# Kernel optimization log

Measured on AMD Instinct MI355X. Metric: run time of the kernel, lower is better.

Reference implementation:

```python
import jax, jax.numpy as jnp
import numpy as np

BS, S, H, T = 16, 256, 1024, 32  # batch, num entities, hidden, num relation tags
N_TAGS = 7


def setup_inputs() -> dict:
    key = jax.random.key(0)
    k0, k1, k2, k3 = jax.random.split(key, 4)
    seq_embedding = jax.random.normal(k0, (BS, H), dtype=jnp.float32)
    entities_embeddings = jax.random.normal(k1, (BS, S, H), dtype=jnp.float32)
    entities_tags = jax.random.randint(k2, (BS, S), 0, N_TAGS)
    # relation_classifier: Linear(3*H -> T)
    W = jax.random.normal(k3, (T, 3 * H), dtype=jnp.float32) * 0.02
    b = jnp.zeros((T,), dtype=jnp.float32)
    return {
        "seq_embedding": seq_embedding,
        "entities_embeddings": entities_embeddings,
        "W": W,
        "b": b,
        "entities_tags": entities_tags,
    }


def reference(seq_embedding, entities_embeddings, W, b, entities_tags):
    # Original (eval mode, dropout=identity):
    #   pred[b,i,j] = W @ concat(E[b,i], E[b,j], S[b]) + bias
    # (arg1/arg2/all_seq linears and tag embeddings are dead code in the
    #  original forward: their outputs are never used.)
    # Decompose W = [W1 | W2 | W3] along the feature axis; mathematically
    # identical to materializing the (bs,S,S,3H) concat tensor.
    h = entities_embeddings.shape[-1]
    W1, W2, W3 = W[:, :h], W[:, h:2 * h], W[:, 2 * h:]
    p1 = jnp.einsum('bih,th->bit', entities_embeddings, W1)  # arg1 contribution
    p2 = jnp.einsum('bjh,th->bjt', entities_embeddings, W2)  # arg2 contribution
    ps = seq_embedding @ W3.T + b                             # seq + bias
    # (bs, S, S, T)
    return p1[:, :, None, :] + p2[:, None, :, :] + ps[:, None, None, :]
```

## Files before the change

kernel.cpp:

```cpp
#include <hip/hip_runtime.h>

#define BS 16
#define S  256
#define H  1024
#define T  32

#define PS_OFF 0
#define P1_OFF 512
#define P2_OFF (P1_OFF + BS * S * T)

typedef __bf16 bf16x8 __attribute__((ext_vector_type(8)));
typedef float  f32x4  __attribute__((ext_vector_type(4)));

__device__ inline bf16x8 to_bf8(float4 lo, float4 hi) {
    bf16x8 r;
    r[0] = (__bf16)lo.x; r[1] = (__bf16)lo.y; r[2] = (__bf16)lo.z; r[3] = (__bf16)lo.w;
    r[4] = (__bf16)hi.x; r[5] = (__bf16)hi.y; r[6] = (__bf16)hi.z; r[7] = (__bf16)hi.w;
    return r;
}

__global__ __launch_bounds__(256) void gemm_ps(
    const float* __restrict__ seq, const float* __restrict__ E,
    const float* __restrict__ W, const float* __restrict__ bias,
    float* __restrict__ ws)
{
    const int tid = threadIdx.x;
    const int lane = tid & 63, wv = tid >> 6;

    if (blockIdx.x < 128) {
        float* ps = ws + PS_OFF;
        const int o = blockIdx.x * 4 + wv;
        const int bb = o >> 5, t = o & 31;
        const float4* sp = (const float4*)(seq + (size_t)bb * H) + lane * 4;
        const float4* wp = (const float4*)(W + (size_t)t * (3 * H) + 2 * H) + lane * 4;
        float acc = 0.f;
        #pragma unroll
        for (int k = 0; k < 4; ++k) {
            float4 a = sp[k], w = wp[k];
            acc += a.x * w.x + a.y * w.y + a.z * w.z + a.w * w.w;
        }
        #pragma unroll
        for (int m = 32; m >= 1; m >>= 1) acc += __shfl_xor(acc, m);
        if (lane == 0) ps[o] = acc + bias[t];
        return;
    }

    __shared__ __align__(16) __bf16 Ebf[16][1032];
    __shared__ __align__(16) float  pacc[4][16][64];

    const int m0 = (blockIdx.x - 128) * 16;

    #pragma unroll
    for (int i = 0; i < 8; ++i) {
        int f = tid + i * 256;
        int row = f >> 7, c8 = f & 127;
        const float4* src = (const float4*)(E + (size_t)(m0 + row) * H + c8 * 8);
        *(bf16x8*)&Ebf[row][c8 * 8] = to_bf8(src[0], src[1]);
    }

    const int kc = wv * 256;
    const int ksub = (lane >> 4) * 8;
    bf16x8 bf[32];
    #pragma unroll
    for (int nt = 0; nt < 4; ++nt) {
        const int col = nt * 16 + (lane & 15);
        const float* wb = W + (size_t)(col & 31) * (3 * H)
                            + ((col >= 32) ? H : 0) + kc + ksub;
        #pragma unroll
        for (int s = 0; s < 8; ++s)
            bf[nt * 8 + s] = to_bf8(*(const float4*)(wb + s * 32),
                                    *(const float4*)(wb + s * 32 + 4));
    }

    __syncthreads();

    f32x4 acc[4] = {{0.f,0.f,0.f,0.f},{0.f,0.f,0.f,0.f},
                    {0.f,0.f,0.f,0.f},{0.f,0.f,0.f,0.f}};
    const int erow = lane & 15;
    #pragma unroll
    for (int s = 0; s < 8; ++s) {
        bf16x8 a = *(const bf16x8*)&Ebf[erow][kc + s * 32 + ksub];
        acc[0] = __builtin_amdgcn_mfma_f32_16x16x32_bf16(a, bf[s],      acc[0], 0, 0, 0);
        acc[1] = __builtin_amdgcn_mfma_f32_16x16x32_bf16(a, bf[8 + s],  acc[1], 0, 0, 0);
        acc[2] = __builtin_amdgcn_mfma_f32_16x16x32_bf16(a, bf[16 + s], acc[2], 0, 0, 0);
        acc[3] = __builtin_amdgcn_mfma_f32_16x16x32_bf16(a, bf[24 + s], acc[3], 0, 0, 0);
    }

    const int prow = (lane >> 4) * 4;
    #pragma unroll
    for (int nt = 0; nt < 4; ++nt)
        #pragma unroll
        for (int r = 0; r < 4; ++r)
            pacc[wv][prow + r][nt * 16 + (lane & 15)] = acc[nt][r];

    __syncthreads();

    const int col = tid & 63;
    const int r0 = tid >> 6;
    #pragma unroll
    for (int rr = 0; rr < 4; ++rr) {
        const int row = r0 + rr * 4;
        float v = (pacc[0][row][col] + pacc[1][row][col])
                + (pacc[2][row][col] + pacc[3][row][col]);
        if (col < 32) (ws + P1_OFF)[(size_t)(m0 + row) * T + col] = v;
        else          (ws + P2_OFF)[(size_t)(m0 + row) * T + (col - 32)] = v;
    }
}

__global__ __launch_bounds__(256) void bcast_add(
    const float* __restrict__ ws, float* __restrict__ out)
{
    const int blk = blockIdx.x;
    const int b = blk >> 8, i = blk & 255;
    const int tid = threadIdx.x;

    __shared__ __align__(16) float s1[32];
    if (tid < 32)
        s1[tid] = (ws + P1_OFF)[(size_t)(b * S + i) * T + tid]
                + (ws + PS_OFF)[b * T + tid];
    __syncthreads();

    const float4 s = *(const float4*)&s1[(tid & 7) * 4];
    const float4* p2v = (const float4*)(ws + P2_OFF) + (size_t)b * (S * T / 4);
    float4* ov = (float4*)out + (size_t)(b * S + i) * (S * T / 4);

    #pragma unroll
    for (int k = tid; k < S * T / 4; k += 256) {
        float4 v = p2v[k];
        float4 r;
        r.x = v.x + s.x; r.y = v.y + s.y; r.z = v.z + s.z; r.w = v.w + s.w;
        ov[k] = r;
    }
}

extern "C" void kernel_launch(void* const* d_in, const int* in_sizes, int n_in,
                              void* d_out, int out_size, void* d_ws, size_t ws_size,
                              hipStream_t stream)
{
    const float* seq  = (const float*)d_in[0];
    const float* E    = (const float*)d_in[1];
    const float* W    = (const float*)d_in[2];
    const float* bias = (const float*)d_in[3];
    float* out = (float*)d_out;
    float* ws  = (float*)d_ws;

    gemm_ps<<<384, 256, 0, stream>>>(seq, E, W, bias, ws);
    bcast_add<<<BS * S, 256, 0, stream>>>(ws, out);
}
```

Baseline: 43.66 us.

## Widen GEMM blocks to 16 waves, drop shared staging, use nontemporal stores

The projection kernel now runs 1024-thread blocks: 16 waves split the work as 4 K-slices by 4 column groups, so each wave holds only 8 B fragments and issues a single MFMA chain, which cuts register pressure. The grid shrinks to 288 blocks. The broadcast kernel reads its row vector straight from global memory instead of staging it through shared memory with a barrier, and writes the large output with nontemporal stores to avoid polluting the cache. Larger blocks may reduce occupancy flexibility, and the output write dominates the total time, so the gain is likely small.

Result: faster. 40.68 us (-6.8%).

```diff
diff --git a/kernel.cpp b/kernel.cpp
--- a/kernel.cpp
+++ b/kernel.cpp
@@ -11,6 +11,7 @@
 
 typedef __bf16 bf16x8 __attribute__((ext_vector_type(8)));
 typedef float  f32x4  __attribute__((ext_vector_type(4)));
+typedef float  f4n    __attribute__((ext_vector_type(4)));
 
 __device__ inline bf16x8 to_bf8(float4 lo, float4 hi) {
     bf16x8 r;
@@ -19,7 +20,7 @@
     return r;
 }
 
-__global__ __launch_bounds__(256) void gemm_ps(
+__global__ __launch_bounds__(1024) void gemm_ps(
     const float* __restrict__ seq, const float* __restrict__ E,
     const float* __restrict__ W, const float* __restrict__ bias,
     float* __restrict__ ws)
@@ -27,9 +28,9 @@
     const int tid = threadIdx.x;
     const int lane = tid & 63, wv = tid >> 6;
 
-    if (blockIdx.x < 128) {
+    if (blockIdx.x < 32) {
         float* ps = ws + PS_OFF;
-        const int o = blockIdx.x * 4 + wv;
+        const int o = blockIdx.x * 16 + wv;
         const int bb = o >> 5, t = o & 31;
         const float4* sp = (const float4*)(seq + (size_t)bb * H) + lane * 4;
         const float4* wp = (const float4*)(W + (size_t)t * (3 * H) + 2 * H) + lane * 4;
@@ -48,62 +49,51 @@
     __shared__ __align__(16) __bf16 Ebf[16][1032];
     __shared__ __align__(16) float  pacc[4][16][64];
 
-    const int m0 = (blockIdx.x - 128) * 16;
+    const int m0 = (blockIdx.x - 32) * 16;
+    const int ks = wv >> 2;
+    const int cg = wv & 3;
+    const int kbeg = ks * 256;
+
+    const int col = cg * 16 + (lane & 15);
+    const int ksub = (lane >> 4) * 8;
+    const float* wbase = W + (size_t)(col & 31) * (3 * H)
+                           + ((col >= 32) ? H : 0) + kbeg + ksub;
+    bf16x8 bfrag[8];
+    #pragma unroll
+    for (int s = 0; s < 8; ++s)
+        bfrag[s] = to_bf8(*(const float4*)(wbase + s * 32),
+                          *(const float4*)(wbase + s * 32 + 4));
 
     #pragma unroll
-    for (int i = 0; i < 8; ++i) {
-        int f = tid + i * 256;
-        int row = f >> 7, c8 = f & 127;
+    for (int i = 0; i < 2; ++i) {
+        int c = tid + i * 1024;
+        int row = c >> 7, c8 = c & 127;
         const float4* src = (const float4*)(E + (size_t)(m0 + row) * H + c8 * 8);
         *(bf16x8*)&Ebf[row][c8 * 8] = to_bf8(src[0], src[1]);
     }
+    __syncthreads();
 
-    const int kc = wv * 256;
-    const int ksub = (lane >> 4) * 8;
-    bf16x8 bf[32];
+    f32x4 acc = {0.f, 0.f, 0.f, 0.f};
+    const int erow = lane & 15;
+    const int kof = kbeg + ksub;
     #pragma unroll
-    for (int nt = 0; nt < 4; ++nt) {
-        const int col = nt * 16 + (lane & 15);
-        const float* wb = W + (size_t)(col & 31) * (3 * H)
-                            + ((col >= 32) ? H : 0) + kc + ksub;
-        #pragma unroll
-        for (int s = 0; s < 8; ++s)
-            bf[nt * 8 + s] = to_bf8(*(const float4*)(wb + s * 32),
-                                    *(const float4*)(wb + s * 32 + 4));
+    for (int s = 0; s < 8; ++s) {
+        bf16x8 a = *(const bf16x8*)&Ebf[erow][kof + s * 32];
+        acc = __builtin_amdgcn_mfma_f32_16x16x32_bf16(a, bfrag[s], acc, 0, 0, 0);
     }
 
+    const int orow = (lane >> 4) * 4;
+    #pragma unroll
+    for (int r = 0; r < 4; ++r)
+        pacc[ks][orow + r][col] = acc[r];
     __syncthreads();
 
-    f32x4 acc[4] = {{0.f,0.f,0.f,0.f},{0.f,0.f,0.f,0.f},
-                    {0.f,0.f,0.f,0.f},{0.f,0.f,0.f,0.f}};
-    const int erow = lane & 15;
-    #pragma unroll
-    for (int s = 0; s < 8; ++s) {
-        bf16x8 a = *(const bf16x8*)&Ebf[erow][kc + s * 32 + ksub];
-        acc[0] = __builtin_amdgcn_mfma_f32_16x16x32_bf16(a, bf[s],      acc[0], 0, 0, 0);
-        acc[1] = __builtin_amdgcn_mfma_f32_16x16x32_bf16(a, bf[8 + s],  acc[1], 0, 0, 0);
-        acc[2] = __builtin_amdgcn_mfma_f32_16x16x32_bf16(a, bf[16 + s], acc[2], 0, 0, 0);
-        acc[3] = __builtin_amdgcn_mfma_f32_16x16x32_bf16(a, bf[24 + s], acc[3], 0, 0, 0);
-    }
-
-    const int prow = (lane >> 4) * 4;
-    #pragma unroll
-    for (int nt = 0; nt < 4; ++nt)
-        #pragma unroll
-        for (int r = 0; r < 4; ++r)
-            pacc[wv][prow + r][nt * 16 + (lane & 15)] = acc[nt][r];
-
-    __syncthreads();
-
-    const int col = tid & 63;
-    const int r0 = tid >> 6;
-    #pragma unroll
-    for (int rr = 0; rr < 4; ++rr) {
-        const int row = r0 + rr * 4;
-        float v = (pacc[0][row][col] + pacc[1][row][col])
-                + (pacc[2][row][col] + pacc[3][row][col]);
-        if (col < 32) (ws + P1_OFF)[(size_t)(m0 + row) * T + col] = v;
-        else          (ws + P2_OFF)[(size_t)(m0 + row) * T + (col - 32)] = v;
+    {
+        const int row = tid >> 6, c = tid & 63;
+        float v = (pacc[0][row][c] + pacc[1][row][c])
+                + (pacc[2][row][c] + pacc[3][row][c]);
+        if (c < 32) (ws + P1_OFF)[(size_t)(m0 + row) * T + c] = v;
+        else        (ws + P2_OFF)[(size_t)(m0 + row) * T + (c - 32)] = v;
     }
 }
 
@@ -114,22 +104,22 @@
     const int b = blk >> 8, i = blk & 255;
     const int tid = threadIdx.x;
 
-    __shared__ __align__(16) float s1[32];
-    if (tid < 32)
-        s1[tid] = (ws + P1_OFF)[(size_t)(b * S + i) * T + tid]
-                + (ws + PS_OFF)[b * T + tid];
-    __syncthreads();
+    const float4 s1v = *(const float4*)((ws + P1_OFF)
+                       + (size_t)(b * S + i) * T + (tid & 7) * 4);
+    const float4 psv = *(const float4*)((ws + PS_OFF) + b * T + (tid & 7) * 4);
+    float4 s;
+    s.x = s1v.x + psv.x; s.y = s1v.y + psv.y;
+    s.z = s1v.z + psv.z; s.w = s1v.w + psv.w;
 
-    const float4 s = *(const float4*)&s1[(tid & 7) * 4];
     const float4* p2v = (const float4*)(ws + P2_OFF) + (size_t)b * (S * T / 4);
     float4* ov = (float4*)out + (size_t)(b * S + i) * (S * T / 4);
 
     #pragma unroll
     for (int k = tid; k < S * T / 4; k += 256) {
         float4 v = p2v[k];
-        float4 r;
+        f4n r;
         r.x = v.x + s.x; r.y = v.y + s.y; r.z = v.z + s.z; r.w = v.w + s.w;
-        ov[k] = r;
+        __builtin_nontemporal_store(r, (f4n*)&ov[k]);
     }
 }
 
@@ -144,6 +134,6 @@
     float* out = (float*)d_out;
     float* ws  = (float*)d_ws;
 
-    gemm_ps<<<384, 256, 0, stream>>>(seq, E, W, bias, ws);
+    gemm_ps<<<288, 1024, 0, stream>>>(seq, E, W, bias, ws);
     bcast_add<<<BS * S, 256, 0, stream>>>(ws, out);
 }
```

## Fuse projection GEMM into tiled broadcast-add kernel, dropping p1/p2 workspace round trip

Applied to the files above, without the earlier changes.

Replaces the GEMM-then-broadcast pair with a small ps kernel plus a tiled kernel in which each block recomputes the p1 rows for 16 i and the p2 rows for 64 j of one batch with MFMA. It then writes the 16x64x32 output tile straight from shared memory. This removes the p1/p2 workspace writes and the re-reads of p2 across the broadcast. In exchange E and W are re-read and recomputed redundantly across tiles (each E row is converted about 4x, W is loaded per block), adding extra GEMM work before the store-bound output phase.

New measurement: 135.6 us. 211% more time.

```diff
diff --git a/kernel.cpp b/kernel.cpp
--- a/kernel.cpp
+++ b/kernel.cpp
@@ -4,10 +4,10 @@
 #define S  256
 #define H  1024
 #define T  32
+#define IT 16
+#define JT 64
 
 #define PS_OFF 0
-#define P1_OFF 512
-#define P2_OFF (P1_OFF + BS * S * T)
 
 typedef __bf16 bf16x8 __attribute__((ext_vector_type(8)));
 typedef float  f32x4  __attribute__((ext_vector_type(4)));
@@ -19,117 +19,116 @@
     return r;
 }
 
-__global__ __launch_bounds__(256) void gemm_ps(
-    const float* __restrict__ seq, const float* __restrict__ E,
-    const float* __restrict__ W, const float* __restrict__ bias,
-    float* __restrict__ ws)
+__global__ __launch_bounds__(256) void ps_kernel(
+    const float* __restrict__ seq, const float* __restrict__ W,
+    const float* __restrict__ bias, float* __restrict__ ws)
 {
+    const int lane = threadIdx.x & 63, wv = threadIdx.x >> 6;
+    float* ps = ws + PS_OFF;
+    const int o = blockIdx.x * 4 + wv;
+    const int bb = o >> 5, t = o & 31;
+    const float4* sp = (const float4*)(seq + (size_t)bb * H) + lane * 4;
+    const float4* wp = (const float4*)(W + (size_t)t * (3 * H) + 2 * H) + lane * 4;
+    float acc = 0.f;
+    #pragma unroll
+    for (int k = 0; k < 4; ++k) {
+        float4 a = sp[k], w = wp[k];
+        acc += a.x * w.x + a.y * w.y + a.z * w.z + a.w * w.w;
+    }
+    #pragma unroll
+    for (int m = 32; m >= 1; m >>= 1) acc += __shfl_xor(acc, m);
+    if (lane == 0) ps[o] = acc + bias[t];
+}
+
+__global__ __launch_bounds__(256) void tile_kernel(
+    const float* __restrict__ E, const float* __restrict__ W,
+    const float* __restrict__ ws, float* __restrict__ out)
+{
+    __shared__ __align__(16) __bf16 Es[80][264];
+
     const int tid = threadIdx.x;
-    const int lane = tid & 63, wv = tid >> 6;
+    const int lane = tid & 63, w = tid >> 6;
+    const int blk = blockIdx.x;
+    const int b = blk >> 6, it = (blk >> 2) & 15, jt = blk & 3;
+    const int i0 = it * IT, j0 = jt * JT;
 
-    if (blockIdx.x < 128) {
-        float* ps = ws + PS_OFF;
-        const int o = blockIdx.x * 4 + wv;
-        const int bb = o >> 5, t = o & 31;
-        const float4* sp = (const float4*)(seq + (size_t)bb * H) + lane * 4;
-        const float4* wp = (const float4*)(W + (size_t)t * (3 * H) + 2 * H) + lane * 4;
-        float acc = 0.f;
+    const int col  = lane & 15;
+    const int ksub = (lane >> 4) * 8;
+
+    f32x4 ap2[2] = {{0.f,0.f,0.f,0.f},{0.f,0.f,0.f,0.f}};
+    f32x4 ap1[2] = {{0.f,0.f,0.f,0.f},{0.f,0.f,0.f,0.f}};
+
+    for (int kc = 0; kc < 4; ++kc) {
+        if (kc) __syncthreads();
+        for (int c = tid; c < 80 * 32; c += 256) {
+            int row = c >> 5, ch = c & 31;
+            int grow = (row < IT) ? (i0 + row) : (j0 + row - IT);
+            const float4* src = (const float4*)(E + ((size_t)(b * S + grow)) * H
+                                                + kc * 256 + ch * 8);
+            *(bf16x8*)&Es[row][ch * 8] = to_bf8(src[0], src[1]);
+        }
+        __syncthreads();
+
+        const __bf16* arow2 = &Es[IT + w * 16 + col][ksub];
         #pragma unroll
-        for (int k = 0; k < 4; ++k) {
-            float4 a = sp[k], w = wp[k];
-            acc += a.x * w.x + a.y * w.y + a.z * w.z + a.w * w.w;
+        for (int s = 0; s < 8; ++s) {
+            bf16x8 a = *(const bf16x8*)(arow2 + s * 32);
+            #pragma unroll
+            for (int nt = 0; nt < 2; ++nt) {
+                const float* wb = W + (size_t)(nt * 16 + col) * (3 * H) + H
+                                    + kc * 256 + s * 32 + ksub;
+                bf16x8 bf = to_bf8(*(const float4*)wb, *(const float4*)(wb + 4));
+                ap2[nt] = __builtin_amdgcn_mfma_f32_16x16x32_bf16(a, bf, ap2[nt], 0, 0, 0);
+            }
         }
+        const __bf16* arow1 = &Es[col][ksub];
         #pragma unroll
-        for (int m = 32; m >= 1; m >>= 1) acc += __shfl_xor(acc, m);
-        if (lane == 0) ps[o] = acc + bias[t];
-        return;
+        for (int sp = 0; sp < 2; ++sp) {
+            const int s = w * 2 + sp;
+            bf16x8 a = *(const bf16x8*)(arow1 + s * 32);
+            #pragma unroll
+            for (int nt = 0; nt < 2; ++nt) {
+                const float* wb = W + (size_t)(nt * 16 + col) * (3 * H)
+                                    + kc * 256 + s * 32 + ksub;
+                bf16x8 bf = to_bf8(*(const float4*)wb, *(const float4*)(wb + 4));
+                ap1[nt] = __builtin_amdgcn_mfma_f32_16x16x32_bf16(a, bf, ap1[nt], 0, 0, 0);
+            }
+        }
     }
+    __syncthreads();
 
-    __shared__ __align__(16) __bf16 Ebf[16][1032];
-    __shared__ __align__(16) float  pacc[4][16][64];
+    float* fl = (float*)&Es[0][0];
+    const int drow = (lane >> 4) * 4;
+    #pragma unroll
+    for (int nt = 0; nt < 2; ++nt)
+        #pragma unroll
+        for (int r = 0; r < 4; ++r) {
+            fl[w * 512 + (drow + r) * 32 + nt * 16 + col]        = ap1[nt][r];
+            fl[2048 + w * 576 + (drow + r) * 36 + nt * 16 + col] = ap2[nt][r];
+        }
+    __syncthreads();
 
-    const int m0 = (blockIdx.x - 128) * 16;
+    const float* psv = ws + PS_OFF + b * T;
+    for (int e = tid; e < IT * T; e += 256) {
+        int t = e & 31;
+        fl[4352 + e] = ((fl[e] + fl[512 + e]) + (fl[1024 + e] + fl[1536 + e])) + psv[t];
+    }
+    __syncthreads();
 
     #pragma unroll
-    for (int i = 0; i < 8; ++i) {
-        int f = tid + i * 256;
-        int row = f >> 7, c8 = f & 127;
-        const float4* src = (const float4*)(E + (size_t)(m0 + row) * H + c8 * 8);
-        *(bf16x8*)&Ebf[row][c8 * 8] = to_bf8(src[0], src[1]);
-    }
-
-    const int kc = wv * 256;
-    const int ksub = (lane >> 4) * 8;
-    bf16x8 bf[32];
-    #pragma unroll
-    for (int nt = 0; nt < 4; ++nt) {
-        const int col = nt * 16 + (lane & 15);
-        const float* wb = W + (size_t)(col & 31) * (3 * H)
-                            + ((col >= 32) ? H : 0) + kc + ksub;
+    for (int i = 0; i < IT; ++i) {
+        const size_t rb4 = (((size_t)(b * S + i0 + i) * S + j0 + w * 16) * T) >> 2;
         #pragma unroll
-        for (int s = 0; s < 8; ++s)
-            bf[nt * 8 + s] = to_bf8(*(const float4*)(wb + s * 32),
-                                    *(const float4*)(wb + s * 32 + 4));
-    }
-
-    __syncthreads();
-
-    f32x4 acc[4] = {{0.f,0.f,0.f,0.f},{0.f,0.f,0.f,0.f},
-                    {0.f,0.f,0.f,0.f},{0.f,0.f,0.f,0.f}};
-    const int erow = lane & 15;
-    #pragma unroll
-    for (int s = 0; s < 8; ++s) {
-        bf16x8 a = *(const bf16x8*)&Ebf[erow][kc + s * 32 + ksub];
-        acc[0] = __builtin_amdgcn_mfma_f32_16x16x32_bf16(a, bf[s],      acc[0], 0, 0, 0);
-        acc[1] = __builtin_amdgcn_mfma_f32_16x16x32_bf16(a, bf[8 + s],  acc[1], 0, 0, 0);
-        acc[2] = __builtin_amdgcn_mfma_f32_16x16x32_bf16(a, bf[16 + s], acc[2], 0, 0, 0);
-        acc[3] = __builtin_amdgcn_mfma_f32_16x16x32_bf16(a, bf[24 + s], acc[3], 0, 0, 0);
-    }
-
-    const int prow = (lane >> 4) * 4;
-    #pragma unroll
-    for (int nt = 0; nt < 4; ++nt)
-        #pragma unroll
-        for (int r = 0; r < 4; ++r)
-            pacc[wv][prow + r][nt * 16 + (lane & 15)] = acc[nt][r];
-
-    __syncthreads();
-
-    const int col = tid & 63;
-    const int r0 = tid >> 6;
-    #pragma unroll
-    for (int rr = 0; rr < 4; ++rr) {
-        const int row = r0 + rr * 4;
-        float v = (pacc[0][row][col] + pacc[1][row][col])
-                + (pacc[2][row][col] + pacc[3][row][col]);
-        if (col < 32) (ws + P1_OFF)[(size_t)(m0 + row) * T + col] = v;
-        else          (ws + P2_OFF)[(size_t)(m0 + row) * T + (col - 32)] = v;
-    }
-}
-
-__global__ __launch_bounds__(256) void bcast_add(
-    const float* __restrict__ ws, float* __restrict__ out)
-{
-    const int blk = blockIdx.x;
-    const int b = blk >> 8, i = blk & 255;
-    const int tid = threadIdx.x;
-
-    __shared__ __align__(16) float s1[32];
-    if (tid < 32)
-        s1[tid] = (ws + P1_OFF)[(size_t)(b * S + i) * T + tid]
-                + (ws + PS_OFF)[b * T + tid];
-    __syncthreads();
-
-    const float4 s = *(const float4*)&s1[(tid & 7) * 4];
-    const float4* p2v = (const float4*)(ws + P2_OFF) + (size_t)b * (S * T / 4);
-    float4* ov = (float4*)out + (size_t)(b * S + i) * (S * T / 4);
-
-    #pragma unroll
-    for (int k = tid; k < S * T / 4; k += 256) {
-        float4 v = p2v[k];
-        float4 r;
-        r.x = v.x + s.x; r.y = v.y + s.y; r.z = v.z + s.z; r.w = v.w + s.w;
-        ov[k] = r;
+        for (int h = 0; h < 2; ++h) {
+            const int f = lane + h * 64;
+            const int jl = f >> 3, t4 = f & 7;
+            float4 pv = *(const float4*)&fl[2048 + w * 576 + jl * 36 + t4 * 4];
+            float4 sv = *(const float4*)&fl[4352 + i * 32 + t4 * 4];
+            float4 r;
+            r.x = pv.x + sv.x; r.y = pv.y + sv.y;
+            r.z = pv.z + sv.z; r.w = pv.w + sv.w;
+            ((float4*)out)[rb4 + f] = r;
+        }
     }
 }
 
@@ -144,6 +143,6 @@
     float* out = (float*)d_out;
     float* ws  = (float*)d_ws;
 
-    gemm_ps<<<384, 256, 0, stream>>>(seq, E, W, bias, ws);
-    bcast_add<<<BS * S, 256, 0, stream>>>(ws, out);
+    ps_kernel<<<128, 256, 0, stream>>>(seq, W, bias, ws);
+    tile_kernel<<<1024, 256, 0, stream>>>(E, W, ws, out);
 }
```
